# Optimization experiments

Measured on AMD Instinct MI355X. Metric: run time of the kernel, lower is better.

The kernel has to match this reference:

```python
import jax, jax.numpy as jnp
import numpy as np
from jax import lax

K = 20
EPS = 1e-5
SLOPE = 0.2


def knn_idx(x, k):
    # x: [B, C, N] -> idx [B, N, k] of nearest neighbors (incl. self)
    inner = jnp.einsum('bcn,bcm->bnm', x, x)
    sq = jnp.sum(x * x, axis=1)                      # [B, N]
    neg_d = -(sq[:, :, None] + sq[:, None, :] - 2.0 * inner)
    _, idx = lax.top_k(neg_d, k)
    return idx


def graph_feature(x, idx):
    # x: [B, C, N], idx: [B, N, k] -> [B, 2C, N, k]
    B = x.shape[0]
    xt = jnp.transpose(x, (0, 2, 1))                 # [B, N, C]
    neigh = xt[jnp.arange(B)[:, None, None], idx]    # [B, N, k, C]
    center = jnp.broadcast_to(xt[:, :, None, :], neigh.shape)
    feat = jnp.concatenate([neigh - center, center], axis=-1)  # [B, N, k, 2C]
    return jnp.transpose(feat, (0, 3, 1, 2))         # [B, 2C, N, k]


def conv_bn_lrelu(feat, W, gamma, beta):
    # 1x1 Conv2d (no bias) + eval-mode BN (mean=0, var=1) + LeakyReLU(0.2)
    y = jnp.einsum('oc,bcnk->bonk', W, feat)
    scale = gamma / jnp.sqrt(1.0 + EPS)
    y = y * scale[None, :, None, None] + beta[None, :, None, None]
    return jnp.where(y >= 0, y, SLOPE * y)


def setup_inputs() -> dict:
    key = jax.random.key(0)
    ks = jax.random.split(key, 16)
    B, N, emb = 4, 2048, 1024
    d = {'x': jax.random.normal(ks[0], (B, 3, N), dtype=jnp.float32)}
    dims = [(64, 6), (64, 128), (128, 128), (256, 256), (emb, 256)]
    for i, (o, c) in enumerate(dims):
        d[f'W{i+1}'] = jax.random.normal(ks[1 + i], (o, c), dtype=jnp.float32) * (1.0 / np.sqrt(c))
        d[f'g{i+1}'] = 1.0 + 0.1 * jax.random.normal(ks[6 + i], (o,), dtype=jnp.float32)
        d[f'b{i+1}'] = 0.1 * jax.random.normal(ks[11 + i], (o,), dtype=jnp.float32)
    return d


def reference(x, W1, W2, W3, W4, W5, g1, g2, g3, g4, g5, b1, b2, b3, b4, b5):
    # EdgeConv block 1
    f = graph_feature(x, knn_idx(x, K))              # [B, 6, N, k]
    x1 = jnp.max(conv_bn_lrelu(f, W1, g1, b1), axis=-1)   # [B, 64, N]
    # EdgeConv block 2
    f = graph_feature(x1, knn_idx(x1, K))            # [B, 128, N, k]
    x2 = jnp.max(conv_bn_lrelu(f, W2, g2, b2), axis=-1)   # [B, 64, N]
    # EdgeConv block 3
    f = graph_feature(x2, knn_idx(x2, K))            # [B, 128, N, k]
    x3 = jnp.max(conv_bn_lrelu(f, W3, g3, b3), axis=-1)   # [B, 128, N]
    # EdgeConv block 4
    f = graph_feature(x3, knn_idx(x3, K))            # [B, 256, N, k]
    x4 = jnp.max(conv_bn_lrelu(f, W4, g4, b4), axis=-1)   # [B, 256, N]
    # conv5 (1x1 over points) + global max pool
    x5 = conv_bn_lrelu(x4[:, :, :, None], W5, g5, b5)     # [B, emb, N, 1]
    return jnp.max(x5[..., 0], axis=-1)              # [B, emb]
```

## Files before the change

### kernel.cpp

```cpp
#include <hip/hip_runtime.h>
#include <math.h>

#define BB 4
#define NN 2048
#define KK 20
#define INFPK 0xFFFFFFFFFFFFFFFFull

static __device__ __forceinline__ float lrelu(float z) {
    return z >= 0.f ? z : 0.2f * z;
}

template<int CTRL>
static __device__ __forceinline__ unsigned long long dpp_min64_step(unsigned long long v) {
    unsigned lo = (unsigned)__builtin_amdgcn_update_dpp(
        (int)0xFFFFFFFFu, (int)(unsigned)v, CTRL, 0xF, 0xF, false);
    unsigned hi = (unsigned)__builtin_amdgcn_update_dpp(
        (int)0xFFFFFFFFu, (int)(unsigned)(v >> 32), CTRL, 0xF, 0xF, false);
    unsigned long long t = ((unsigned long long)hi << 32) | lo;
    return t < v ? t : v;
}
static __device__ __forceinline__ unsigned long long wave_min64_bcast(unsigned long long v) {
    v = dpp_min64_step<0x111>(v);
    v = dpp_min64_step<0x112>(v);
    v = dpp_min64_step<0x114>(v);
    v = dpp_min64_step<0x118>(v);
    v = dpp_min64_step<0x142>(v);
    v = dpp_min64_step<0x143>(v);
    unsigned lo = (unsigned)__builtin_amdgcn_readlane((int)(unsigned)v, 63);
    unsigned hi = (unsigned)__builtin_amdgcn_readlane((int)(unsigned)(v >> 32), 63);
    return ((unsigned long long)hi << 32) | lo;
}

template<int C>
__global__ __launch_bounds__(256) void sq_kernel(const float* __restrict__ x,
                                                 float* __restrict__ sq) {
    int i = blockIdx.x * 256 + threadIdx.x;
    if (i >= BB * NN) return;
    int b = i / NN, n = i - b * NN;
    const float* xb = x + (size_t)b * C * NN + n;
    float s = 0.f;
    #pragma unroll
    for (int c = 0; c < C; ++c) {
        float v = xb[(size_t)c * NN];
        s = fmaf(v, v, s);
    }
    sq[i] = s;
}

template<int C>
__global__ __launch_bounds__(256, 4) void knn_kernel(const float* __restrict__ x,
                                                     const float* __restrict__ sq,
                                                     int* __restrict__ idx) {
    const int QT = 4;
    __shared__ unsigned dl[QT][NN];
    __shared__ float xq[QT][C];
    __shared__ float sqq[QT];
    int blk = blockIdx.x;
    int b = blk / (NN / QT);
    int q0 = (blk - b * (NN / QT)) * QT;
    int t = threadIdx.x;
    int lane = t & 63, wid = t >> 6;

    const float* xb = x + (size_t)b * C * NN;
    for (int e = t; e < QT * C; e += 256) {
        int q = e / C, c = e - q * C;
        xq[q][c] = xb[(size_t)c * NN + q0 + q];
    }
    if (t < QT) sqq[t] = sq[b * NN + q0 + t];
    __syncthreads();

    float acc[QT][8];
    #pragma unroll
    for (int q = 0; q < QT; ++q)
        #pragma unroll
        for (int s = 0; s < 8; ++s) acc[q][s] = 0.f;

    for (int c = 0; c < C; ++c) {
        float xj[8];
        #pragma unroll
        for (int s = 0; s < 8; ++s) xj[s] = xb[(size_t)c * NN + t + s * 256];
        #pragma unroll
        for (int q = 0; q < QT; ++q) {
            float xqc = xq[q][c];
            #pragma unroll
            for (int s = 0; s < 8; ++s) acc[q][s] = fmaf(xqc, xj[s], acc[q][s]);
        }
    }
    float sqj[8];
    #pragma unroll
    for (int s = 0; s < 8; ++s) sqj[s] = sq[b * NN + t + s * 256];

    #pragma unroll
    for (int q = 0; q < QT; ++q) {
        float sqi = sqq[q];
        #pragma unroll
        for (int s = 0; s < 8; ++s) {
            float d = sqi + sqj[s] - 2.f * acc[q][s];
            unsigned u = __float_as_uint(d);
            unsigned key = u ^ ((unsigned)((int)u >> 31) | 0x80000000u);
            int j = s * 256 + t;
            int w = (j & ~31) | ((((j >> 2) ^ (j >> 5)) & 7) << 2) | (j & 3);
            dl[q][w] = key;
        }
    }
    __syncthreads();

    unsigned* dq = &dl[wid][0];
    int r7 = lane & 7;
    int lanebase = lane << 5;

    unsigned long long h0 = INFPK, h1 = INFPK, h2 = INFPK, h3 = INFPK;

#define PK_INS(KEY, LO) {                                                     \
        unsigned long long v =                                                \
            ((unsigned long long)(KEY) << 12) | (unsigned)(lanebase + (LO));  \
        if (v < h3) {                                                         \
            unsigned long long nh3 = h2 > v ? h2 : v;                         \
            unsigned long long t2  = h2 < v ? h2 : v;                         \
            unsigned long long nh2 = h1 > t2 ? h1 : t2;                       \
            unsigned long long t1  = h1 < v ? h1 : v;                         \
            unsigned long long nh1 = h0 > t1 ? h0 : t1;                       \
            unsigned long long nh0 = h0 < v ? h0 : v;                         \
            h0 = nh0; h1 = nh1; h2 = nh2; h3 = nh3;                           \
        } }
#define PK_INS_THR(KEY, LO) {                                                 \
        unsigned long long v =                                                \
            ((unsigned long long)(KEY) << 12) | (unsigned)(lanebase + (LO));  \
        if (v > thr && v < h3) {                                              \
            unsigned long long nh3 = h2 > v ? h2 : v;                         \
            unsigned long long t2  = h2 < v ? h2 : v;                         \
            unsigned long long nh2 = h1 > t2 ? h1 : t2;                       \
            unsigned long long t1  = h1 < v ? h1 : v;                         \
            unsigned long long nh1 = h0 > t1 ? h0 : t1;                       \
            unsigned long long nh0 = h0 < v ? h0 : v;                         \
            h0 = nh0; h1 = nh1; h2 = nh2; h3 = nh3;                           \
        } }
#define CHUNK_RD(c) uint4 V##c = *(const uint4*)(dq + lanebase + (((c) ^ r7) << 2));
#define CHUNK_INS(c)     { PK_INS(V##c.x, 4*(c)+0) PK_INS(V##c.y, 4*(c)+1)        \
                           PK_INS(V##c.z, 4*(c)+2) PK_INS(V##c.w, 4*(c)+3) }
#define CHUNK_INS_THR(c) { PK_INS_THR(V##c.x, 4*(c)+0) PK_INS_THR(V##c.y, 4*(c)+1) \
                           PK_INS_THR(V##c.z, 4*(c)+2) PK_INS_THR(V##c.w, 4*(c)+3) }

    {
        CHUNK_RD(0) CHUNK_RD(1) CHUNK_RD(2) CHUNK_RD(3)
        CHUNK_RD(4) CHUNK_RD(5) CHUNK_RD(6) CHUNK_RD(7)
        CHUNK_INS(0) CHUNK_INS(1) CHUNK_INS(2) CHUNK_INS(3)
        CHUNK_INS(4) CHUNK_INS(5) CHUNK_INS(6) CHUNK_INS(7)
    }

    int* orow = idx + (size_t)(b * NN + q0 + wid) * KK;
    unsigned long long thr = 0;
    int popped = 0;
    #pragma unroll 1
    for (int rr = 0; rr < KK; ++rr) {
        unsigned long long g = wave_min64_bcast(h0);
        if (lane == 0) orow[rr] = (int)(g & 0xFFFu);
        if (h0 == g) {
            thr = g;
            ++popped;
            h0 = h1; h1 = h2; h2 = h3; h3 = INFPK;
            if (h0 == INFPK && popped < 32) {
                CHUNK_RD(0) CHUNK_RD(1) CHUNK_RD(2) CHUNK_RD(3)
                CHUNK_RD(4) CHUNK_RD(5) CHUNK_RD(6) CHUNK_RD(7)
                CHUNK_INS_THR(0) CHUNK_INS_THR(1) CHUNK_INS_THR(2) CHUNK_INS_THR(3)
                CHUNK_INS_THR(4) CHUNK_INS_THR(5) CHUNK_INS_THR(6) CHUNK_INS_THR(7)
            }
        }
    }
#undef PK_INS
#undef PK_INS_THR
#undef CHUNK_RD
#undef CHUNK_INS
#undef CHUNK_INS_THR
}

template<int C, int OT>
__global__ __launch_bounds__(256) void pt_kernel(const float* __restrict__ x,
                                                 const float* __restrict__ W,
                                                 float* __restrict__ p,
                                                 float* __restrict__ tt,
                                                 int O) {
    const int NB = NN / 256;
    int blk = blockIdx.x;
    int nb = blk % NB;
    int rest = blk / NB;
    int nob = O / OT;
    int ob = rest % nob;
    int b = rest / nob;
    int t = threadIdx.x;
    int n = nb * 256 + t;
    __shared__ float wn[OT][C], wd[OT][C];
    for (int e = t; e < OT * C; e += 256) {
        int o = e / C, c = e - o * C;
        float a = W[(size_t)(ob * OT + o) * (2 * C) + c];
        float b2 = W[(size_t)(ob * OT + o) * (2 * C) + C + c];
        wn[o][c] = a;
        wd[o][c] = b2 - a;
    }
    __syncthreads();
    float ap[OT], at[OT];
    #pragma unroll
    for (int o = 0; o < OT; ++o) { ap[o] = 0.f; at[o] = 0.f; }
    const float* xb = x + (size_t)b * C * NN + n;
    for (int c = 0; c < C; ++c) {
        float xv = xb[(size_t)c * NN];
        #pragma unroll
        for (int o = 0; o < OT; ++o) {
            ap[o] = fmaf(wn[o][c], xv, ap[o]);
            at[o] = fmaf(wd[o][c], xv, at[o]);
        }
    }
    size_t base = ((size_t)b * O + ob * OT) * NN + n;
    #pragma unroll
    for (int o = 0; o < OT; ++o) {
        p[base + (size_t)o * NN] = ap[o];
        tt[base + (size_t)o * NN] = at[o];
    }
}

__global__ __launch_bounds__(256) void edge_kernel(const float* __restrict__ p,
                                                   const float* __restrict__ tt,
                                                   const int* __restrict__ idx,
                                                   const float* __restrict__ g,
                                                   const float* __restrict__ be,
                                                   float* __restrict__ out, int O) {
    int b = blockIdx.x / O, o = blockIdx.x - b * O;
    __shared__ float pl[NN];
    const float* pr = p + ((size_t)b * O + o) * NN;
    for (int e = threadIdx.x * 4; e < NN; e += 1024)
        *(float4*)&pl[e] = *(const float4*)&pr[e];
    __syncthreads();
    float scale = g[o] / sqrtf(1.f + 1e-5f);
    float beta = be[o];
    const float* tr = tt + ((size_t)b * O + o) * NN;
    float* orow = out + ((size_t)b * O + o) * NN;
    for (int i = threadIdx.x; i < NN; i += 256) {
        float ti = tr[i];
        const int4* ir4 = (const int4*)(idx + (size_t)(b * NN + i) * KK);
        int4 w0 = ir4[0], w1 = ir4[1], w2 = ir4[2], w3 = ir4[3], w4 = ir4[4];
        float m = -__builtin_inff();
        int js[20] = {w0.x, w0.y, w0.z, w0.w, w1.x, w1.y, w1.z, w1.w,
                      w2.x, w2.y, w2.z, w2.w, w3.x, w3.y, w3.z, w3.w,
                      w4.x, w4.y, w4.z, w4.w};
        #pragma unroll
        for (int k = 0; k < KK; ++k) {
            float y = pl[js[k]] + ti;
            m = fmaxf(m, lrelu(fmaf(scale, y, beta)));
        }
        orow[i] = m;
    }
}

__global__ __launch_bounds__(256) void transpose_kernel(const float* __restrict__ W,
                                                        float* __restrict__ WT) {
    __shared__ float tile[32][33];
    int c0 = blockIdx.x * 32, o0 = blockIdx.y * 32;
    int tx = threadIdx.x, ty = threadIdx.y;
    #pragma unroll
    for (int i = 0; i < 32; i += 8)
        tile[ty + i][tx] = W[(size_t)(o0 + ty + i) * 256 + c0 + tx];
    __syncthreads();
    #pragma unroll
    for (int i = 0; i < 32; i += 8)
        WT[(size_t)(c0 + ty + i) * 1024 + o0 + tx] = tile[tx][ty + i];
}

__global__ __launch_bounds__(256) void final_kernel(const float* __restrict__ x4,
                                                    const float* __restrict__ W5T,
                                                    const float* __restrict__ g,
                                                    const float* __restrict__ be,
                                                    float* __restrict__ partial) {
    const int CC = 256;
    __shared__ float xs[64][64];
    __shared__ float ws[64][64];
    int blk = blockIdx.x;
    int nb = blk & 31;
    int ob = (blk >> 5) & 15;
    int b  = blk >> 9;
    int t = threadIdx.x;
    int tn = t & 15, to = t >> 4;

    float acc[4][4];
    #pragma unroll
    for (int i = 0; i < 4; ++i)
        #pragma unroll
        for (int j = 0; j < 4; ++j) acc[i][j] = 0.f;

    for (int c0 = 0; c0 < CC; c0 += 64) {
        __syncthreads();
        #pragma unroll
        for (int e = t * 4; e < 64 * 64; e += 1024) {
            int c = e >> 6, n = e & 63;
            *(float4*)&xs[c][n] =
                *(const float4*)&x4[((size_t)b * CC + c0 + c) * NN + nb * 64 + n];
        }
        #pragma unroll
        for (int e = t * 4; e < 64 * 64; e += 1024) {
            int c = e >> 6, o = e & 63;
            *(float4*)&ws[c][o] =
                *(const float4*)&W5T[(size_t)(c0 + c) * 1024 + ob * 64 + o];
        }
        __syncthreads();
        for (int c = 0; c < 64; ++c) {
            float4 xv = *(float4*)&xs[c][tn * 4];
            float4 wv = *(float4*)&ws[c][to * 4];
            acc[0][0] = fmaf(wv.x, xv.x, acc[0][0]);
            acc[0][1] = fmaf(wv.x, xv.y, acc[0][1]);
            acc[0][2] = fmaf(wv.x, xv.z, acc[0][2]);
            acc[0][3] = fmaf(wv.x, xv.w, acc[0][3]);
            acc[1][0] = fmaf(wv.y, xv.x, acc[1][0]);
            acc[1][1] = fmaf(wv.y, xv.y, acc[1][1]);
            acc[1][2] = fmaf(wv.y, xv.z, acc[1][2]);
            acc[1][3] = fmaf(wv.y, xv.w, acc[1][3]);
            acc[2][0] = fmaf(wv.z, xv.x, acc[2][0]);
            acc[2][1] = fmaf(wv.z, xv.y, acc[2][1]);
            acc[2][2] = fmaf(wv.z, xv.z, acc[2][2]);
            acc[2][3] = fmaf(wv.z, xv.w, acc[2][3]);
            acc[3][0] = fmaf(wv.w, xv.x, acc[3][0]);
            acc[3][1] = fmaf(wv.w, xv.y, acc[3][1]);
            acc[3][2] = fmaf(wv.w, xv.z, acc[3][2]);
            acc[3][3] = fmaf(wv.w, xv.w, acc[3][3]);
        }
    }

    float rs = 1.f / sqrtf(1.f + 1e-5f);
    #pragma unroll
    for (int i = 0; i < 4; ++i) {
        int o = ob * 64 + to * 4 + i;
        float scale = g[o] * rs, beta = be[o];
        float m = -__builtin_inff();
        #pragma unroll
        for (int j = 0; j < 4; ++j)
            m = fmaxf(m, lrelu(fmaf(scale, acc[i][j], beta)));
        #pragma unroll
        for (int off = 8; off >= 1; off >>= 1)
            m = fmaxf(m, __shfl_xor(m, off));
        if (tn == 0)
            partial[(size_t)(nb * BB + b) * 1024 + o] = m;
    }
}

__global__ __launch_bounds__(256) void reduce32_kernel(const float* __restrict__ partial,
                                                       float* __restrict__ out) {
    int i = blockIdx.x * 256 + threadIdx.x;
    if (i >= BB * 1024) return;
    int b = i >> 10, o = i & 1023;
    float m = -__builtin_inff();
    #pragma unroll
    for (int nb = 0; nb < 32; ++nb)
        m = fmaxf(m, partial[(size_t)(nb * BB + b) * 1024 + o]);
    out[i] = m;
}

extern "C" void kernel_launch(void* const* d_in, const int* in_sizes, int n_in,
                              void* d_out, int out_size, void* d_ws, size_t ws_size,
                              hipStream_t stream) {
    const float* x  = (const float*)d_in[0];
    const float* W1 = (const float*)d_in[1];
    const float* g1 = (const float*)d_in[2];
    const float* b1 = (const float*)d_in[3];
    const float* W2 = (const float*)d_in[4];
    const float* g2 = (const float*)d_in[5];
    const float* b2 = (const float*)d_in[6];
    const float* W3 = (const float*)d_in[7];
    const float* g3 = (const float*)d_in[8];
    const float* b3 = (const float*)d_in[9];
    const float* W4 = (const float*)d_in[10];
    const float* g4 = (const float*)d_in[11];
    const float* b4 = (const float*)d_in[12];
    const float* W5 = (const float*)d_in[13];
    const float* g5 = (const float*)d_in[14];
    const float* b5 = (const float*)d_in[15];

    float* ws = (float*)d_ws;
    float* sq      = ws;
    int*   idx     = (int*)(ws + 8192);
    float* x1      = ws + 8192 + 163840;
    float* x2      = x1 + 524288;
    float* x3      = x2 + 524288;
    float* x4      = x3 + 1048576;
    float* p       = x4 + 2097152;
    float* tt      = p + 2097152;
    float* W5T     = p;
    float* partial = tt;

    dim3 blk(256);

    sq_kernel<3><<<32, blk, 0, stream>>>(x, sq);
    knn_kernel<3><<<BB * (NN / 4), blk, 0, stream>>>(x, sq, idx);
    pt_kernel<3, 16><<<BB * (64 / 16) * (NN / 256), blk, 0, stream>>>(x, W1, p, tt, 64);
    edge_kernel<<<BB * 64, blk, 0, stream>>>(p, tt, idx, g1, b1, x1, 64);

    sq_kernel<64><<<32, blk, 0, stream>>>(x1, sq);
    knn_kernel<64><<<BB * (NN / 4), blk, 0, stream>>>(x1, sq, idx);
    pt_kernel<64, 16><<<BB * (64 / 16) * (NN / 256), blk, 0, stream>>>(x1, W2, p, tt, 64);
    edge_kernel<<<BB * 64, blk, 0, stream>>>(p, tt, idx, g2, b2, x2, 64);

    sq_kernel<64><<<32, blk, 0, stream>>>(x2, sq);
    knn_kernel<64><<<BB * (NN / 4), blk, 0, stream>>>(x2, sq, idx);
    pt_kernel<64, 16><<<BB * (128 / 16) * (NN / 256), blk, 0, stream>>>(x2, W3, p, tt, 128);
    edge_kernel<<<BB * 128, blk, 0, stream>>>(p, tt, idx, g3, b3, x3, 128);

    sq_kernel<128><<<32, blk, 0, stream>>>(x3, sq);
    knn_kernel<128><<<BB * (NN / 4), blk, 0, stream>>>(x3, sq, idx);
    pt_kernel<128, 16><<<BB * (256 / 16) * (NN / 256), blk, 0, stream>>>(x3, W4, p, tt, 256);
    edge_kernel<<<BB * 256, blk, 0, stream>>>(p, tt, idx, g4, b4, x4, 256);

    transpose_kernel<<<dim3(8, 32), dim3(32, 8), 0, stream>>>(W5, W5T);
    final_kernel<<<BB * 16 * 32, blk, 0, stream>>>(x4, W5T, g5, b5, partial);
    reduce32_kernel<<<16, blk, 0, stream>>>(partial, (float*)d_out);
}
```

Before: 588.8 us.

## Process 8 queries per kNN block with 512 threads and float4 loads

The kNN kernel now handles 8 query points per block using 512 threads, which halves the number of blocks and the number of times each candidate column is re-read from global memory. Each thread now owns 4 contiguous candidates, loaded as float4, and writes their keys to shared memory with a single uint4 store using a recomputed swizzle. The trade-off is a larger shared-memory footprint (64 KB per block) and the loss of the explicit 4-blocks-per-CU launch bound, which may lower occupancy during the selection phase. This assumes the unseen selection code, indexed by wave id, handles 8 waves correctly.

```diff
diff --git a/kernel.cpp b/kernel.cpp
--- a/kernel.cpp
+++ b/kernel.cpp
@@ -48,10 +48,10 @@
 }
 
 template<int C>
-__global__ __launch_bounds__(256, 4) void knn_kernel(const float* __restrict__ x,
-                                                     const float* __restrict__ sq,
-                                                     int* __restrict__ idx) {
-    const int QT = 4;
+__global__ __launch_bounds__(512) void knn_kernel(const float* __restrict__ x,
+                                                  const float* __restrict__ sq,
+                                                  int* __restrict__ idx) {
+    const int QT = 8;
     __shared__ unsigned dl[QT][NN];
     __shared__ float xq[QT][C];
     __shared__ float sqq[QT];
@@ -62,46 +62,47 @@
     int lane = t & 63, wid = t >> 6;
 
     const float* xb = x + (size_t)b * C * NN;
-    for (int e = t; e < QT * C; e += 256) {
+    for (int e = t; e < QT * C; e += 512) {
         int q = e / C, c = e - q * C;
         xq[q][c] = xb[(size_t)c * NN + q0 + q];
     }
     if (t < QT) sqq[t] = sq[b * NN + q0 + t];
     __syncthreads();
 
-    float acc[QT][8];
+    float acc[QT][4];
     #pragma unroll
     for (int q = 0; q < QT; ++q)
         #pragma unroll
-        for (int s = 0; s < 8; ++s) acc[q][s] = 0.f;
+        for (int u = 0; u < 4; ++u) acc[q][u] = 0.f;
 
     for (int c = 0; c < C; ++c) {
-        float xj[8];
-        #pragma unroll
-        for (int s = 0; s < 8; ++s) xj[s] = xb[(size_t)c * NN + t + s * 256];
+        float4 xj = *(const float4*)&xb[(size_t)c * NN + 4 * t];
         #pragma unroll
         for (int q = 0; q < QT; ++q) {
             float xqc = xq[q][c];
-            #pragma unroll
-            for (int s = 0; s < 8; ++s) acc[q][s] = fmaf(xqc, xj[s], acc[q][s]);
-        }
-    }
-    float sqj[8];
-    #pragma unroll
-    for (int s = 0; s < 8; ++s) sqj[s] = sq[b * NN + t + s * 256];
-
+            acc[q][0] = fmaf(xqc, xj.x, acc[q][0]);
+            acc[q][1] = fmaf(xqc, xj.y, acc[q][1]);
+            acc[q][2] = fmaf(xqc, xj.z, acc[q][2]);
+            acc[q][3] = fmaf(xqc, xj.w, acc[q][3]);
+        }
+    }
+    float4 sqj = *(const float4*)&sq[b * NN + 4 * t];
+    float sqju[4] = {sqj.x, sqj.y, sqj.z, sqj.w};
+
+    int wbase = ((t >> 3) << 5) | (((t ^ (t >> 3)) & 7) << 2);
     #pragma unroll
     for (int q = 0; q < QT; ++q) {
         float sqi = sqq[q];
-        #pragma unroll
-        for (int s = 0; s < 8; ++s) {
-            float d = sqi + sqj[s] - 2.f * acc[q][s];
-            unsigned u = __float_as_uint(d);
-            unsigned key = u ^ ((unsigned)((int)u >> 31) | 0x80000000u);
-            int j = s * 256 + t;
-            int w = (j & ~31) | ((((j >> 2) ^ (j >> 5)) & 7) << 2) | (j & 3);
-            dl[q][w] = key;
-        }
+        uint4 kv;
+        unsigned ks[4];
+        #pragma unroll
+        for (int u = 0; u < 4; ++u) {
+            float d = sqi + sqju[u] - 2.f * acc[q][u];
+            unsigned v = __float_as_uint(d);
+            ks[u] = v ^ ((unsigned)((int)v >> 31) | 0x80000000u);
+        }
+        kv.x = ks[0]; kv.y = ks[1]; kv.z = ks[2]; kv.w = ks[3];
+        *(uint4*)&dl[q][wbase] = kv;
     }
     __syncthreads();
 
@@ -384,25 +385,25 @@
     float* W5T     = p;
     float* partial = tt;
 
-    dim3 blk(256);
+    dim3 blk(256), kblk(512);
 
     sq_kernel<3><<<32, blk, 0, stream>>>(x, sq);
-    knn_kernel<3><<<BB * (NN / 4), blk, 0, stream>>>(x, sq, idx);
+    knn_kernel<3><<<BB * (NN / 8), kblk, 0, stream>>>(x, sq, idx);
     pt_kernel<3, 16><<<BB * (64 / 16) * (NN / 256), blk, 0, stream>>>(x, W1, p, tt, 64);
     edge_kernel<<<BB * 64, blk, 0, stream>>>(p, tt, idx, g1, b1, x1, 64);
 
     sq_kernel<64><<<32, blk, 0, stream>>>(x1, sq);
-    knn_kernel<64><<<BB * (NN / 4), blk, 0, stream>>>(x1, sq, idx);
+    knn_kernel<64><<<BB * (NN / 8), kblk, 0, stream>>>(x1, sq, idx);
     pt_kernel<64, 16><<<BB * (64 / 16) * (NN / 256), blk, 0, stream>>>(x1, W2, p, tt, 64);
     edge_kernel<<<BB * 64, blk, 0, stream>>>(p, tt, idx, g2, b2, x2, 64);
 
     sq_kernel<64><<<32, blk, 0, stream>>>(x2, sq);
-    knn_kernel<64><<<BB * (NN / 4), blk, 0, stream>>>(x2, sq, idx);
+    knn_kernel<64><<<BB * (NN / 8), kblk, 0, stream>>>(x2, sq, idx);
     pt_kernel<64, 16><<<BB * (128 / 16) * (NN / 256), blk, 0, stream>>>(x2, W3, p, tt, 128);
     edge_kernel<<<BB * 128, blk, 0, stream>>>(p, tt, idx, g3, b3, x3, 128);
 
     sq_kernel<128><<<32, blk, 0, stream>>>(x3, sq);
-    knn_kernel<128><<<BB * (NN / 4), blk, 0, stream>>>(x3, sq, idx);
+    knn_kernel<128><<<BB * (NN / 8), kblk, 0, stream>>>(x3, sq, idx);
     pt_kernel<128, 16><<<BB * (256 / 16) * (NN / 256), blk, 0, stream>>>(x3, W4, p, tt, 256);
     edge_kernel<<<BB * 256, blk, 0, stream>>>(p, tt, idx, g4, b4, x4, 256);
 
```

New measurement: 562.1 us. -4.5%, faster.
